# Kernel tuning notes

Hardware: AMD Instinct MI355X
Metric: run time of the kernel (lower is better)

The kernel has to match this reference:

```python
import jax, jax.numpy as jnp
import numpy as np

CONF_THRES = 0.7
IOU_THRES = 0.45
MAX_DET = 512  # padded per-image candidate count after confidence top-k


def setup_inputs() -> dict:
    key = jax.random.key(0)
    # raw YOLO-style predictions: [B, N, 9] = cx,cy,w,h,obj,cls,pitch,yaw,roll
    pred = jax.random.uniform(key, (64, 100800, 9), dtype=jnp.float32)
    return {"pred": pred}


def _xywh2xyxy(b):
    cx, cy, w, h = b[..., 0], b[..., 1], b[..., 2], b[..., 3]
    return jnp.stack([cx - w * 0.5, cy - h * 0.5, cx + w * 0.5, cy + h * 0.5], axis=-1)


def _pairwise_iou(boxes):
    # boxes: [B, K, 4] in xyxy -> [B, K, K] IoU matrix
    lt = jnp.maximum(boxes[:, :, None, :2], boxes[:, None, :, :2])
    rb = jnp.minimum(boxes[:, :, None, 2:], boxes[:, None, :, 2:])
    wh = jnp.clip(rb - lt, 0.0)
    inter = wh[..., 0] * wh[..., 1]
    area = (boxes[..., 2] - boxes[..., 0]) * (boxes[..., 3] - boxes[..., 1])
    union = area[:, :, None] + area[:, None, :] - inter
    return inter / (union + 1e-7)


def reference(pred):
    """Batched YOLOv5-style NMS (single class) with DirectMHP euler angles.

    Returns [B, MAX_DET, 9]: x1,y1,x2,y2,conf,class,pitch,yaw,roll;
    suppressed / below-threshold slots are zeroed (fixed-shape padding).
    """
    K = MAX_DET
    conf = pred[..., 4] * pred[..., 5]                  # obj * cls prob
    score = jnp.where(conf > CONF_THRES, conf, 0.0)     # threshold filter
    top_scores, idx = jax.lax.top_k(score, K)           # sorted desc, [B, K]

    take = lambda a: jnp.take_along_axis(a, idx[..., None], axis=1)
    boxes = _xywh2xyxy(take(pred[..., :4]))             # [B, K, 4]
    angles = take(pred[..., 6:9])                       # [B, K, 3]

    iou = _pairwise_iou(boxes)                          # [B, K, K]
    keep0 = top_scores > CONF_THRES                     # [B, K]
    rng = jnp.arange(K)

    def body(i, keep):
        # greedy suppression: box i (if still kept) kills later boxes with IoU > thr
        keep_i = jnp.take(keep, i, axis=1)[:, None]     # [B, 1]
        iou_i = jnp.take(iou, i, axis=1)                # [B, K]
        sup = (iou_i > IOU_THRES) & keep_i & (rng > i)[None, :]
        return keep & ~sup

    keep = jax.lax.fori_loop(0, K, body, keep0)

    cls = jnp.zeros_like(top_scores)
    out = jnp.concatenate(
        [boxes, top_scores[..., None], cls[..., None], angles], axis=-1
    )  # [B, K, 9]
    return out * keep[..., None].astype(out.dtype)
```

## Files before the change

### kernel.cpp

```cpp
#include <hip/hip_runtime.h>

#define N_ANCH 100800
#define BATCH 64
#define KTOP 512
#define CNT_STRIDE 64

__global__ void zero_cnt_kernel(int* __restrict__ cnt) {
    if (threadIdx.x < BATCH) cnt[threadIdx.x * CNT_STRIDE] = 0;
}

__global__ void filter_kernel(const float* __restrict__ pred,
                              unsigned long long* __restrict__ cand,
                              int* __restrict__ cnt, int cap) {
    __shared__ float tile[256 * 9];
    __shared__ int s_wbase[4];
    __shared__ int s_blkcnt;
    __shared__ int s_gbase;

    const int b  = blockIdx.y;
    const int r0 = blockIdx.x * 256;
    const int rows = min(256, N_ANCH - r0);
    const size_t base = ((size_t)b * N_ANCH + r0) * 9;

    if (threadIdx.x == 0) s_blkcnt = 0;

    const int nf4 = (rows * 9) >> 2;
    const float4* __restrict__ src = (const float4*)(pred + base);
    float4* dst4 = (float4*)tile;
    for (int f = threadIdx.x; f < nf4; f += 256) dst4[f] = src[f];
    __syncthreads();

    const int t = threadIdx.x;
    const int wid = t >> 6, lane = t & 63;
    bool has = false;
    unsigned long long key = 0;
    if (t < rows) {
        float s = tile[t * 9 + 4] * tile[t * 9 + 5];
        if (s > 0.7f) {
            has = true;
            unsigned int sb = __float_as_uint(s);
            unsigned int gi = (unsigned int)(r0 + t);
            key = ((unsigned long long)sb << 32) | (unsigned long long)(~gi);
        }
    }

    unsigned long long m = __ballot(has);
    if (lane == 0) s_wbase[wid] = atomicAdd(&s_blkcnt, __popcll(m));
    __syncthreads();
    if (t == 0) s_gbase = atomicAdd(&cnt[b * CNT_STRIDE], s_blkcnt);
    __syncthreads();

    if (has) {
        int rank = __popcll(m & ((1ull << lane) - 1ull));
        int pos = s_gbase + s_wbase[wid] + rank;
        if (pos < cap) cand[(size_t)b * cap + pos] = key;
    }
}

__global__ void __launch_bounds__(512)
select_kernel(const float* __restrict__ pred,
              const unsigned long long* __restrict__ cand,
              int* __restrict__ cnt,
              float4* __restrict__ boxesw,
              float* __restrict__ scw,
              float4* __restrict__ angw, int cap) {
#pragma clang fp contract(off)
    __shared__ int hist[2048];
    __shared__ int csf[256];
    __shared__ unsigned long long sel[1024];
    __shared__ int s_bstar, s_nsel;

    const int b = blockIdx.x;
    const int t = threadIdx.x;
    const int c = min(cnt[b * CNT_STRIDE], cap);
    const unsigned long long* __restrict__ cb = cand + (size_t)b * cap;

    for (int i = t; i < 2048; i += 512) hist[i] = 0;
    sel[t] = 0; sel[t + 512] = 0;
    if (t == 0) { s_nsel = 0; s_bstar = 0; }
    __syncthreads();

    for (int i = t; i < c; i += 512) {
        atomicAdd(&hist[(int)((cb[i] >> 44) & 0x7FF)], 1);
    }
    __syncthreads();

    {
        if (t < 256) {
            int s = 0;
            #pragma unroll
            for (int j = 0; j < 8; ++j) s += hist[t * 8 + j];
            csf[t] = s;
        }
        __syncthreads();
        for (int off = 1; off < 256; off <<= 1) {
            int v2 = 0;
            if (t < 256) v2 = csf[t] + ((t + off < 256) ? csf[t + off] : 0);
            __syncthreads();
            if (t < 256) csf[t] = v2;
            __syncthreads();
        }
        if (t < 256) {
            int cs_t  = csf[t];
            int cs_t1 = (t == 255) ? 0 : csf[t + 1];
            if (cs_t >= KTOP && cs_t1 < KTOP) {
                int cum = cs_t1, bstar = t * 8;
                for (int j = 7; j >= 0; --j) {
                    cum += hist[t * 8 + j];
                    if (cum >= KTOP) { bstar = t * 8 + j; break; }
                }
                s_bstar = bstar;
            }
        }
        __syncthreads();
    }

    const int bstar = s_bstar;
    for (int i = t; i < c; i += 512) {
        unsigned long long k = cb[i];
        if ((int)((k >> 44) & 0x7FF) >= bstar) {
            int p = atomicAdd(&s_nsel, 1);
            if (p < 1024) sel[p] = k;
        }
    }
    __syncthreads();
    const int v = min(s_nsel, KTOP);

    {
        const int l = t & 63;
        const int w = t >> 6;
        const int ia = (w << 7) + l;
        const int ib = ia + 64;
        unsigned long long a = sel[ia];
        unsigned long long bq = sel[ib];

        #pragma unroll
        for (int k = 2; k <= 128; k <<= 1) {
            #pragma unroll
            for (int j = k >> 1; j >= 1; j >>= 1) {
                if (j == 64) {
                    bool desc = ((ia & k) == 0);
                    unsigned long long mx = (a > bq) ? a : bq;
                    unsigned long long mn = (a > bq) ? bq : a;
                    a = desc ? mx : mn;
                    bq = desc ? mn : mx;
                } else {
                    unsigned long long pa = __shfl_xor(a, j);
                    unsigned long long pb = __shfl_xor(bq, j);
                    bool keepmax_a = (((l & j) == 0) == ((ia & k) == 0));
                    bool keepmax_b = (((l & j) == 0) == ((ib & k) == 0));
                    a  = keepmax_a ? ((a  > pa) ? a  : pa) : ((a  > pa) ? pa : a );
                    bq = keepmax_b ? ((bq > pb) ? bq : pb) : ((bq > pb) ? pb : bq);
                }
            }
        }

        #pragma unroll
        for (int k = 256; k <= 1024; k <<= 1) {
            sel[ia] = a; sel[ib] = bq;
            __syncthreads();
            for (int j = k >> 1; j >= 128; j >>= 1) {
                int i0 = ((t & ~(j - 1)) << 1) | (t & (j - 1));
                int i1 = i0 | j;
                unsigned long long x = sel[i0], y = sel[i1];
                bool up = ((i0 & k) == 0);
                if ((x < y) == up) { sel[i0] = y; sel[i1] = x; }
                __syncthreads();
            }
            a = sel[ia]; bq = sel[ib];
            #pragma unroll
            for (int j = 64; j >= 1; j >>= 1) {
                if (j == 64) {
                    bool desc = ((ia & k) == 0);
                    unsigned long long mx = (a > bq) ? a : bq;
                    unsigned long long mn = (a > bq) ? bq : a;
                    a = desc ? mx : mn;
                    bq = desc ? mn : mx;
                } else {
                    unsigned long long pa = __shfl_xor(a, j);
                    unsigned long long pb = __shfl_xor(bq, j);
                    bool keepmax_a = (((l & j) == 0) == ((ia & k) == 0));
                    bool keepmax_b = (((l & j) == 0) == ((ib & k) == 0));
                    a  = keepmax_a ? ((a  > pa) ? a  : pa) : ((a  > pa) ? pa : a );
                    bq = keepmax_b ? ((bq > pb) ? bq : pb) : ((bq > pb) ? pb : bq);
                }
            }
        }
        sel[ia] = a; sel[ib] = bq;
        __syncthreads();
    }

    {
        int s = t;
        float4 bx = make_float4(0.f, 0.f, 0.f, 0.f);
        float4 an = make_float4(0.f, 0.f, 0.f, 0.f);
        float scv = 0.f;
        if (s < v) {
            unsigned long long k = sel[s];
            scv = __uint_as_float((unsigned int)(k >> 32));
            int gid = (int)(~(unsigned int)(k & 0xFFFFFFFFull));
            const float* row = pred + ((size_t)b * N_ANCH + gid) * 9;
            float cx = row[0], cy = row[1], w = row[2], h = row[3];
            float hw = w * 0.5f, hh = h * 0.5f;
            bx = make_float4(cx - hw, cy - hh, cx + hw, cy + hh);
            an = make_float4(row[6], row[7], row[8], 0.f);
        }
        boxesw[(size_t)b * KTOP + s] = bx;
        scw[(size_t)b * KTOP + s] = scv;
        angw[(size_t)b * KTOP + s] = an;
        if (t == 0) cnt[b * CNT_STRIDE + 1] = v;
    }
}

__global__ void __launch_bounds__(256)
iou_kernel(const float4* __restrict__ boxesw,
           unsigned long long* __restrict__ mskw) {
#pragma clang fp contract(off)
    __shared__ float4 bxs[KTOP];

    const int w = blockIdx.x;
    const int b = blockIdx.y;
    const int t = threadIdx.x;

    bxs[t]       = boxesw[(size_t)b * KTOP + t];
    bxs[t + 256] = boxesw[(size_t)b * KTOP + t + 256];
    __syncthreads();

    const int j0 = w << 6;
    #pragma unroll
    for (int rep = 0; rep < 2; ++rep) {
        const int i = t + (rep << 8);
        float4 bi = bxs[i];
        float ai = (bi.z - bi.x) * (bi.w - bi.y);
        unsigned long long mword = 0;
        if (j0 + 63 > i) {
            #pragma unroll 8
            for (int jj = 0; jj < 64; ++jj) {
                float4 bj = bxs[j0 + jj];
                float xx1 = fmaxf(bi.x, bj.x);
                float yy1 = fmaxf(bi.y, bj.y);
                float xx2 = fminf(bi.z, bj.z);
                float yy2 = fminf(bi.w, bj.w);
                float ww = fmaxf(xx2 - xx1, 0.f);
                float hh = fmaxf(yy2 - yy1, 0.f);
                float inter = ww * hh;
                float aj = (bj.z - bj.x) * (bj.w - bj.y);
                float uni = ai + aj - inter;
                float iou = inter / (uni + 1e-7f);
                mword |= (unsigned long long)(iou > 0.45f) << jj;
            }
            if (j0 <= i) mword &= (~0ull) << (i - j0 + 1);
        }
        mskw[(((size_t)b << 3) + w) * KTOP + i] = mword;
    }
}

__global__ void __launch_bounds__(512)
suppress_kernel(const float4* __restrict__ boxesw,
                const float* __restrict__ scw,
                const float4* __restrict__ angw,
                const unsigned long long* __restrict__ mskw,
                const int* __restrict__ cnt,
                float* __restrict__ out) {
    __shared__ unsigned long long mlds[8 * 516];
    __shared__ unsigned long long rmw_s[8];

    const int b = blockIdx.x;
    const int t = threadIdx.x;
    const int v = cnt[b * CNT_STRIDE + 1];

    #pragma unroll
    for (int w = 0; w < 8; ++w)
        mlds[w * 516 + t] = mskw[(((size_t)b << 3) + w) * KTOP + t];
    __syncthreads();

    if (t < 64) {
        unsigned long long rm[8] = {0, 0, 0, 0, 0, 0, 0, 0};
        for (int w = 0; w < 8 && (w << 6) < v; ++w) {
            int rem = v - (w << 6);
            unsigned long long valid = (rem >= 64) ? ~0ull : ((1ull << rem) - 1ull);
            unsigned long long alive = ~rm[w] & valid;
            while (alive) {
                int bit = __ffsll(alive) - 1;
                int i = (w << 6) + bit;
                #pragma unroll
                for (int u = 0; u < 8; ++u) rm[u] |= mlds[u * 516 + i];
                alive = ~rm[w] & valid;
                alive &= (bit == 63) ? 0ull : (~0ull << (bit + 1));
            }
        }
        if (t < 8) rmw_s[t] = rm[t];
    }
    __syncthreads();

    {
        int s = t;
        float scv = scw[(size_t)b * KTOP + s];
        bool keep = (scv > 0.7f) && !((rmw_s[s >> 6] >> (s & 63)) & 1ull);
        float* o = out + ((size_t)b * KTOP + s) * 9;
        if (keep) {
            float4 bx = boxesw[(size_t)b * KTOP + s];
            float4 an = angw[(size_t)b * KTOP + s];
            o[0] = bx.x; o[1] = bx.y; o[2] = bx.z; o[3] = bx.w;
            o[4] = scv;  o[5] = 0.f;
            o[6] = an.x; o[7] = an.y; o[8] = an.z;
        } else {
            o[0] = 0.f; o[1] = 0.f; o[2] = 0.f; o[3] = 0.f;
            o[4] = 0.f; o[5] = 0.f; o[6] = 0.f; o[7] = 0.f; o[8] = 0.f;
        }
    }
}

extern "C" void kernel_launch(void* const* d_in, const int* in_sizes, int n_in,
                              void* d_out, int out_size, void* d_ws, size_t ws_size,
                              hipStream_t stream) {
    const float* pred = (const float*)d_in[0];
    float* out = (float*)d_out;
    char* ws = (char*)d_ws;

    int* cnt = (int*)ws;
    size_t off = (size_t)BATCH * CNT_STRIDE * 4;
    float4* boxesw = (float4*)(ws + off); off += (size_t)BATCH * KTOP * sizeof(float4);
    float*  scw    = (float*)(ws + off);  off += (size_t)BATCH * KTOP * sizeof(float);
    float4* angw   = (float4*)(ws + off); off += (size_t)BATCH * KTOP * sizeof(float4);
    unsigned long long* mskw = (unsigned long long*)(ws + off);
    off += (size_t)BATCH * 8 * KTOP * sizeof(unsigned long long);
    unsigned long long* cand = (unsigned long long*)(ws + off);

    int cap = 8192;
    size_t need = off + (size_t)BATCH * cap * sizeof(unsigned long long);
    if (ws_size < need) {
        cap = (int)((ws_size > off ? (ws_size - off) : 0) /
                    (BATCH * sizeof(unsigned long long)));
    }

    zero_cnt_kernel<<<1, 64, 0, stream>>>(cnt);

    dim3 g1((N_ANCH + 255) / 256, BATCH);
    filter_kernel<<<g1, 256, 0, stream>>>(pred, cand, cnt, cap);

    select_kernel<<<BATCH, 512, 0, stream>>>(pred, cand, cnt, boxesw, scw, angw, cap);

    iou_kernel<<<dim3(8, BATCH), 256, 0, stream>>>(boxesw, mskw);

    suppress_kernel<<<BATCH, 512, 0, stream>>>(boxesw, scw, angw, mskw, cnt, out);
}
```

Baseline: 383.5 us.

## Fuse select, IoU and suppression kernels into one per-image kernel

Merges the select, IoU-mask and suppression kernels into a single kernel per image that keeps boxes and the suppression mask in shared memory. This removes two kernel launches and the global-memory round trips for boxes, scores, angles and masks. The IoU work now runs on only 64 blocks instead of 512, so there is less parallelism for that stage. Shared-memory use per block also grows, which may lower occupancy.

Result: slower. 399.9 us (+4.3%).

```diff
diff --git a/kernel.cpp b/kernel.cpp
--- a/kernel.cpp
+++ b/kernel.cpp
@@ -58,16 +58,17 @@
 }
 
 __global__ void __launch_bounds__(512)
-select_kernel(const float* __restrict__ pred,
-              const unsigned long long* __restrict__ cand,
-              int* __restrict__ cnt,
-              float4* __restrict__ boxesw,
-              float* __restrict__ scw,
-              float4* __restrict__ angw, int cap) {
+fused_kernel(const float* __restrict__ pred,
+             const unsigned long long* __restrict__ cand,
+             const int* __restrict__ cnt,
+             float* __restrict__ out, int cap) {
 #pragma clang fp contract(off)
     __shared__ int hist[2048];
     __shared__ int csf[256];
     __shared__ unsigned long long sel[1024];
+    __shared__ float4 boxes[KTOP];
+    __shared__ unsigned long long msk[KTOP][9];
+    __shared__ unsigned long long rmw_s[8];
     __shared__ int s_bstar, s_nsel;
 
     const int b = blockIdx.x;
@@ -190,11 +191,11 @@
         __syncthreads();
     }
 
+    float scv = 0.f;
+    float an0 = 0.f, an1 = 0.f, an2 = 0.f;
     {
         int s = t;
         float4 bx = make_float4(0.f, 0.f, 0.f, 0.f);
-        float4 an = make_float4(0.f, 0.f, 0.f, 0.f);
-        float scv = 0.f;
         if (s < v) {
             unsigned long long k = sel[s];
             scv = __uint_as_float((unsigned int)(k >> 32));
@@ -203,75 +204,41 @@
             float cx = row[0], cy = row[1], w = row[2], h = row[3];
             float hw = w * 0.5f, hh = h * 0.5f;
             bx = make_float4(cx - hw, cy - hh, cx + hw, cy + hh);
-            an = make_float4(row[6], row[7], row[8], 0.f);
-        }
-        boxesw[(size_t)b * KTOP + s] = bx;
-        scw[(size_t)b * KTOP + s] = scv;
-        angw[(size_t)b * KTOP + s] = an;
-        if (t == 0) cnt[b * CNT_STRIDE + 1] = v;
-    }
-}
-
-__global__ void __launch_bounds__(256)
-iou_kernel(const float4* __restrict__ boxesw,
-           unsigned long long* __restrict__ mskw) {
-#pragma clang fp contract(off)
-    __shared__ float4 bxs[KTOP];
-
-    const int w = blockIdx.x;
-    const int b = blockIdx.y;
-    const int t = threadIdx.x;
-
-    bxs[t]       = boxesw[(size_t)b * KTOP + t];
-    bxs[t + 256] = boxesw[(size_t)b * KTOP + t + 256];
-    __syncthreads();
-
-    const int j0 = w << 6;
-    #pragma unroll
-    for (int rep = 0; rep < 2; ++rep) {
-        const int i = t + (rep << 8);
-        float4 bi = bxs[i];
+            an0 = row[6]; an1 = row[7]; an2 = row[8];
+        }
+        boxes[s] = bx;
+    }
+    __syncthreads();
+
+    {
+        const int i = t;
+        float4 bi = boxes[i];
         float ai = (bi.z - bi.x) * (bi.w - bi.y);
-        unsigned long long mword = 0;
-        if (j0 + 63 > i) {
-            #pragma unroll 8
-            for (int jj = 0; jj < 64; ++jj) {
-                float4 bj = bxs[j0 + jj];
-                float xx1 = fmaxf(bi.x, bj.x);
-                float yy1 = fmaxf(bi.y, bj.y);
-                float xx2 = fminf(bi.z, bj.z);
-                float yy2 = fminf(bi.w, bj.w);
-                float ww = fmaxf(xx2 - xx1, 0.f);
-                float hh = fmaxf(yy2 - yy1, 0.f);
-                float inter = ww * hh;
-                float aj = (bj.z - bj.x) * (bj.w - bj.y);
-                float uni = ai + aj - inter;
-                float iou = inter / (uni + 1e-7f);
-                mword |= (unsigned long long)(iou > 0.45f) << jj;
-            }
-            if (j0 <= i) mword &= (~0ull) << (i - j0 + 1);
-        }
-        mskw[(((size_t)b << 3) + w) * KTOP + i] = mword;
-    }
-}
-
-__global__ void __launch_bounds__(512)
-suppress_kernel(const float4* __restrict__ boxesw,
-                const float* __restrict__ scw,
-                const float4* __restrict__ angw,
-                const unsigned long long* __restrict__ mskw,
-                const int* __restrict__ cnt,
-                float* __restrict__ out) {
-    __shared__ unsigned long long mlds[8 * 516];
-    __shared__ unsigned long long rmw_s[8];
-
-    const int b = blockIdx.x;
-    const int t = threadIdx.x;
-    const int v = cnt[b * CNT_STRIDE + 1];
-
-    #pragma unroll
-    for (int w = 0; w < 8; ++w)
-        mlds[w * 516 + t] = mskw[(((size_t)b << 3) + w) * KTOP + t];
+        #pragma unroll
+        for (int w = 0; w < 8; ++w) {
+            int j0 = w << 6;
+            unsigned long long mword = 0;
+            if (j0 + 63 > i) {
+                #pragma unroll 8
+                for (int jj = 0; jj < 64; ++jj) {
+                    float4 bj = boxes[j0 + jj];
+                    float xx1 = fmaxf(bi.x, bj.x);
+                    float yy1 = fmaxf(bi.y, bj.y);
+                    float xx2 = fminf(bi.z, bj.z);
+                    float yy2 = fminf(bi.w, bj.w);
+                    float ww = fmaxf(xx2 - xx1, 0.f);
+                    float hh = fmaxf(yy2 - yy1, 0.f);
+                    float inter = ww * hh;
+                    float aj = (bj.z - bj.x) * (bj.w - bj.y);
+                    float uni = ai + aj - inter;
+                    float iou = inter / (uni + 1e-7f);
+                    mword |= (unsigned long long)(iou > 0.45f) << jj;
+                }
+                if (j0 <= i) mword &= (~0ull) << (i - j0 + 1);
+            }
+            msk[i][w] = mword;
+        }
+    }
     __syncthreads();
 
     if (t < 64) {
@@ -284,7 +251,7 @@
                 int bit = __ffsll(alive) - 1;
                 int i = (w << 6) + bit;
                 #pragma unroll
-                for (int u = 0; u < 8; ++u) rm[u] |= mlds[u * 516 + i];
+                for (int u = 0; u < 8; ++u) rm[u] |= msk[i][u];
                 alive = ~rm[w] & valid;
                 alive &= (bit == 63) ? 0ull : (~0ull << (bit + 1));
             }
@@ -295,15 +262,13 @@
 
     {
         int s = t;
-        float scv = scw[(size_t)b * KTOP + s];
         bool keep = (scv > 0.7f) && !((rmw_s[s >> 6] >> (s & 63)) & 1ull);
         float* o = out + ((size_t)b * KTOP + s) * 9;
         if (keep) {
-            float4 bx = boxesw[(size_t)b * KTOP + s];
-            float4 an = angw[(size_t)b * KTOP + s];
+            float4 bx = boxes[s];
             o[0] = bx.x; o[1] = bx.y; o[2] = bx.z; o[3] = bx.w;
             o[4] = scv;  o[5] = 0.f;
-            o[6] = an.x; o[7] = an.y; o[8] = an.z;
+            o[6] = an0;  o[7] = an1;  o[8] = an2;
         } else {
             o[0] = 0.f; o[1] = 0.f; o[2] = 0.f; o[3] = 0.f;
             o[4] = 0.f; o[5] = 0.f; o[6] = 0.f; o[7] = 0.f; o[8] = 0.f;
@@ -320,11 +285,6 @@
 
     int* cnt = (int*)ws;
     size_t off = (size_t)BATCH * CNT_STRIDE * 4;
-    float4* boxesw = (float4*)(ws + off); off += (size_t)BATCH * KTOP * sizeof(float4);
-    float*  scw    = (float*)(ws + off);  off += (size_t)BATCH * KTOP * sizeof(float);
-    float4* angw   = (float4*)(ws + off); off += (size_t)BATCH * KTOP * sizeof(float4);
-    unsigned long long* mskw = (unsigned long long*)(ws + off);
-    off += (size_t)BATCH * 8 * KTOP * sizeof(unsigned long long);
     unsigned long long* cand = (unsigned long long*)(ws + off);
 
     int cap = 8192;
@@ -339,9 +299,5 @@
     dim3 g1((N_ANCH + 255) / 256, BATCH);
     filter_kernel<<<g1, 256, 0, stream>>>(pred, cand, cnt, cap);
 
-    select_kernel<<<BATCH, 512, 0, stream>>>(pred, cand, cnt, boxesw, scw, angw, cap);
-
-    iou_kernel<<<dim3(8, BATCH), 256, 0, stream>>>(boxesw, mskw);
-
-    suppress_kernel<<<BATCH, 512, 0, stream>>>(boxesw, scw, angw, mskw, cnt, out);
+    fused_kernel<<<BATCH, 512, 0, stream>>>(pred, cand, cnt, out, cap);
 }
```
